# Kernel tuning notes

Hardware: AMD Instinct MI355X
Metric: run time of the kernel (lower is better)

The kernel has to match this reference:

```python
import jax, jax.numpy as jnp
import numpy as np

LATENT_DIM = 16
NUM_REPLICATES = 10
NUM_STEPS = 10
DT = 0.01
# second-order term index pairs (i <= j), matching standard SINDy library ordering
_TRIU_I, _TRIU_J = np.triu_indices(LATENT_DIM)


def sindy_library(z):
    """z: [..., d] -> Theta: [..., 1 + d + d(d+1)/2 + d] (poly_order=2, include_sine=True)."""
    ones = jnp.ones(z.shape[:-1] + (1,), dtype=z.dtype)
    quad = z[..., _TRIU_I] * z[..., _TRIU_J]  # [..., 136]
    return jnp.concatenate([ones, z, quad, jnp.sin(z)], axis=-1)  # [..., 169]


def setup_inputs() -> dict:
    key = jax.random.key(0)
    k1, k2 = jax.random.split(key)
    h_t = jax.random.normal(k1, (50000, LATENT_DIM), dtype=jnp.float32)
    # torch.nn.init.normal_(coefficients, mean=0.0, std=0.001)
    coefficients = jax.random.normal(k2, (NUM_REPLICATES, 169, LATENT_DIM), dtype=jnp.float32) * 0.001
    coefficient_mask = jnp.ones((NUM_REPLICATES, 169, LATENT_DIM), dtype=jnp.float32)
    return {"h_t": h_t, "coefficients": coefficients, "coefficient_mask": coefficient_mask}


def reference(h_t, coefficients, coefficient_mask):
    # ht_replicates = h_t.unsqueeze(1).repeat(1, num_replicates, 1)
    h_rep = jnp.broadcast_to(h_t[:, None, :], (h_t.shape[0], NUM_REPLICATES, LATENT_DIM))
    masked_coeff = coefficients * coefficient_mask  # [r, l, d]
    # 10 sequential Euler integration steps (E_SINDy.forward)
    for _ in range(NUM_STEPS):
        theta = sindy_library(h_rep)  # [n, r, 169]
        h_rep = h_rep + jnp.einsum('nrl,rld->nrd', theta, masked_coeff) * DT
    return h_rep
```

## Files before the change

kernel.cpp:

```cpp
#include <hip/hip_runtime.h>
#include <hip/hip_bf16.h>
#include <math.h>

#define LATENT 16
#define NREP 10
#define NSTEPS 10
#define NTERMS 169
#define NCHUNK 7
#define DT 0.01f
#define ASCALE 1024.0f
#define INV_ASCALE (1.0f/1024.0f)

#define WS_A_BYTES (NREP * NCHUNK * 64 * 16)
#define WS_C0_OFF  WS_A_BYTES
#define WS_TOTAL   (WS_A_BYTES + NREP * LATENT * 4)

typedef _Float16 h2 __attribute__((ext_vector_type(2)));
typedef _Float16 half8 __attribute__((ext_vector_type(8)));
typedef __fp16 fp16x2 __attribute__((ext_vector_type(2)));
typedef __attribute__((ext_vector_type(4))) float f32x4;
typedef int int4v __attribute__((ext_vector_type(4)));

union FragH  { half8 v; h2 p[4]; int4v i4; };
union FragHE { half8 v; _Float16 e[8]; int4v i4; };

#define SW(x) __builtin_shufflevector((x), (x), 1, 0)

__device__ __forceinline__ h2 pkrtz(float a, float b) {
    fp16x2 r = __builtin_amdgcn_cvt_pkrtz(a, b);
    return __builtin_bit_cast(h2, r);
}

__device__ __forceinline__ h2 shfl_xor_h2(h2 v, int mask) {
    int i = __builtin_bit_cast(int, v);
    return __builtin_bit_cast(h2, __shfl_xor(i, mask));
}

__host__ __device__ constexpr int quadrow(int x, int y) {
    if (x > y) { int t = x; x = y; y = t; }
    return 17 + x * 16 - x * (x - 1) / 2 + (y - x);
}

__host__ __device__ constexpr int krow16(int m, int g) {
    const int sh = 4 * g;
    if (m < 4)  return 1 + (m ^ sh);
    if (m < 8)  return 153 + ((m - 4) ^ sh);
    if (m < 12) { const int a = (m - 8) ^ sh; return quadrow(a, a); }
    if (m < 14) { const int u = m - 12; return quadrow((2*u) ^ sh, (2*u+1) ^ sh); }
    if (m < 30) {
        const int idx = m - 14, rep = idx >> 2, w = idx & 3;
        const int v = 2 * rep + 1;
        const int a = ((w == 1 || w == 3) ? 1 : 0);
        const int b = 2 * v + ((w == 1 || w == 2) ? 1 : 0);
        return quadrow(a ^ sh, b ^ sh);
    }
    if (m < 54) {
        const int idx = m - 30, rep = idx >> 2, w = idx & 3;
        const int u = rep & 1;
        const int v = 2 + 2 * (rep >> 1) + (rep & 1);
        const int d = u ^ v;
        const bool live = (d == 2) ? (g == 0 || g == 2) : (g == 0 || g == 1);
        if (!live) return -1;
        const int a = 2 * u + ((w == 1 || w == 3) ? 1 : 0);
        const int b = 2 * v + ((w == 1 || w == 2) ? 1 : 0);
        return quadrow(a ^ sh, b ^ sh);
    }
    return -1;
}

__global__ __launch_bounds__(448) void pack_A16_kernel(
    const float* __restrict__ coeff, const float* __restrict__ mask, char* __restrict__ ws)
{
    const int r = blockIdx.x;
    const int tid = threadIdx.x;
    const int c = tid >> 6, lane = tid & 63;
    const int d = lane & 15, g = lane >> 4;
    const float* cr = coeff + (size_t)r * NTERMS * LATENT;
    const float* mr = mask  + (size_t)r * NTERMS * LATENT;
    FragHE a;
    for (int e = 0; e < 8; ++e) {
        const int row = krow16(c * 8 + e, g);
        float v = 0.0f;
        if (row >= 0) v = cr[row * LATENT + d] * mr[row * LATENT + d] * (DT * ASCALE);
        a.e[e] = (_Float16)v;
    }
    reinterpret_cast<int4v*>(ws)[((size_t)r * NCHUNK + c) * 64 + lane] = a.i4;

    if (tid < LATENT) {
        float* c0p = reinterpret_cast<float*>(ws + WS_C0_OFF);
        c0p[r * LATENT + tid] = cr[tid] * mr[tid] * (DT * ASCALE);
    }
}

template<bool USE_WS>
__global__ __launch_bounds__(256, 4) void sindy_f16_kernel(
    const float* __restrict__ h_t,
    const float* __restrict__ coeff,
    const float* __restrict__ mask,
    const char* __restrict__ ws,
    float* __restrict__ out,
    int N, int ntiles)
{
    const int lane = threadIdx.x & 63;
    const int wid  = blockIdx.x * 4 + (threadIdx.x >> 6);
    if (wid >= NREP * ntiles) return;
    const int r    = wid / ntiles;
    const int tile = wid % ntiles;

    const int col = lane & 15;
    const int g   = lane >> 4;

    int4v afi[NCHUNK];
    if constexpr (USE_WS) {
        const int4v* wa = reinterpret_cast<const int4v*>(ws);
        #pragma unroll
        for (int c = 0; c < NCHUNK; ++c)
            afi[c] = wa[((size_t)r * NCHUNK + c) * 64 + lane];
    } else {
        const float* cr = coeff + (size_t)r * NTERMS * LATENT;
        const float* mr = mask  + (size_t)r * NTERMS * LATENT;
        #pragma unroll
        for (int c = 0; c < NCHUNK; ++c) {
            FragHE a;
            #pragma unroll
            for (int e = 0; e < 8; ++e) {
                const int row = krow16(c * 8 + e, g);
                float v = 0.0f;
                if (row >= 0) v = cr[row * LATENT + col] * mr[row * LATENT + col] * (DT * ASCALE);
                a.e[e] = (_Float16)v;
            }
            afi[c] = a.i4;
        }
    }

    float c0s[4];
    if constexpr (USE_WS) {
        const float4 v = *reinterpret_cast<const float4*>(
            ws + WS_C0_OFF + ((size_t)r * LATENT + 4 * g) * 4);
        c0s[0] = v.x; c0s[1] = v.y; c0s[2] = v.z; c0s[3] = v.w;
    } else {
        const float* cr = coeff + (size_t)r * NTERMS * LATENT;
        const float* mr = mask  + (size_t)r * NTERMS * LATENT;
        #pragma unroll
        for (int j = 0; j < 4; ++j) {
            const int d2 = 4 * g + j;
            c0s[j] = cr[d2] * mr[d2] * (DT * ASCALE);
        }
    }

    #pragma unroll
    for (int c = 0; c < NCHUNK; ++c) asm volatile("" : "+v"(afi[c]));
    asm volatile("" : "+v"(c0s[0]), "+v"(c0s[1]), "+v"(c0s[2]), "+v"(c0s[3]));

    const int n = tile * 16 + col;
    float h0, h1, h2c, h3c;
    {
        float4 q = make_float4(0.f, 0.f, 0.f, 0.f);
        if (n < N)
            q = *reinterpret_cast<const float4*>(h_t + (size_t)n * LATENT + 4 * g);
        h0 = q.x; h1 = q.y; h2c = q.z; h3c = q.w;
    }

    for (int s = 0; s < NSTEPS; ++s) {
        h2 hp[8];
        hp[0] = pkrtz(h0, h1);
        hp[1] = pkrtz(h2c, h3c);
        #pragma unroll
        for (int u = 1; u < 4; ++u) {
            hp[2 * u]     = shfl_xor_h2(hp[0], 16 * u);
            hp[2 * u + 1] = shfl_xor_h2(hp[1], 16 * u);
        }

        f32x4 acc;
        acc[0] = fmaf(h0,  ASCALE, c0s[0]);
        acc[1] = fmaf(h1,  ASCALE, c0s[1]);
        acc[2] = fmaf(h2c, ASCALE, c0s[2]);
        acc[3] = fmaf(h3c, ASCALE, c0s[3]);

        FragH f;
        #define MM(C) acc = __builtin_amdgcn_mfma_f32_16x16x32_f16( \
            __builtin_bit_cast(half8, afi[C]), f.v, acc, 0, 0, 0);
        f.p[0] = hp[0]; f.p[1] = hp[1];
        f.p[2] = pkrtz(__sinf(h0), __sinf(h1));
        f.p[3] = pkrtz(__sinf(h2c), __sinf(h3c));
        MM(0)
        f.p[0] = hp[0] * hp[0]; f.p[1] = hp[1] * hp[1];
        f.p[2] = pkrtz(h0 * h1, h2c * h3c);
        f.p[3] = hp[0] * hp[1];
        MM(1)
        f.p[0] = hp[0] * SW(hp[1]); f.p[1] = hp[0] * hp[3];
        f.p[2] = hp[0] * SW(hp[3]); f.p[3] = hp[0] * hp[5];
        MM(2)
        f.p[0] = hp[0] * SW(hp[5]); f.p[1] = hp[0] * hp[7];
        f.p[2] = hp[0] * SW(hp[7]); f.p[3] = hp[0] * hp[2];
        MM(3)
        f.p[0] = hp[0] * SW(hp[2]); f.p[1] = hp[1] * hp[3];
        f.p[2] = hp[1] * SW(hp[3]); f.p[3] = hp[0] * hp[4];
        MM(4)
        f.p[0] = hp[0] * SW(hp[4]); f.p[1] = hp[1] * hp[5];
        f.p[2] = hp[1] * SW(hp[5]); f.p[3] = hp[0] * hp[6];
        MM(5)
        f.p[0] = hp[0] * SW(hp[6]); f.p[1] = hp[1] * hp[7];
        f.p[2] = hp[1] * SW(hp[7]); f.p[3] = (h2)(_Float16)0;
        MM(6)
        #undef MM

        h0  = acc[0] * INV_ASCALE;
        h1  = acc[1] * INV_ASCALE;
        h2c = acc[2] * INV_ASCALE;
        h3c = acc[3] * INV_ASCALE;
    }

    if (n < N) {
        float* op = out + ((size_t)n * NREP + r) * LATENT + 4 * g;
        *reinterpret_cast<float4*>(op) = make_float4(h0, h1, h2c, h3c);
    }
}

extern "C" void kernel_launch(void* const* d_in, const int* in_sizes, int n_in,
                              void* d_out, int out_size, void* d_ws, size_t ws_size,
                              hipStream_t stream) {
    const float* h_t   = (const float*)d_in[0];
    const float* coeff = (const float*)d_in[1];
    const float* mask  = (const float*)d_in[2];
    float* out = (float*)d_out;

    const int N = in_sizes[0] / LATENT;
    const int ntiles = (N + 15) / 16;
    const int nwaves = NREP * ntiles;
    const int nblocks = (nwaves + 3) / 4;

    if (ws_size >= (size_t)WS_TOTAL) {
        pack_A16_kernel<<<dim3(NREP), dim3(448), 0, stream>>>(coeff, mask, (char*)d_ws);
        sindy_f16_kernel<true><<<dim3(nblocks), dim3(256), 0, stream>>>(
            h_t, coeff, mask, (const char*)d_ws, out, N, ntiles);
    } else {
        sindy_f16_kernel<false><<<dim3(nblocks), dim3(256), 0, stream>>>(
            h_t, coeff, mask, (const char*)d_ws, out, N, ntiles);
    }
}
```

Before: 55.49 us.

## Process two 16-row tiles per wave to interleave independent MFMA chains

Each wave now handles two tiles of 16 samples that share the same coefficient fragments. It alternates MFMAs between two independent accumulators, so one chain's dependency latency can be covered by the other's work. The launch bound drops from 4 to 3 waves per SIMD to make room for the extra registers. The pack kernel is also split into 70 single-wave blocks. The trade-off is fewer resident waves and half as many waves overall, and the asm barriers that pinned fragments in registers are removed.

Result: no change. 55.18 us (-0.6%).

```diff
diff --git a/kernel.cpp b/kernel.cpp
--- a/kernel.cpp
+++ b/kernel.cpp
@@ -68,12 +68,42 @@
     return -1;
 }
 
-__global__ __launch_bounds__(448) void pack_A16_kernel(
+template<int C>
+__device__ __forceinline__ half8 buildf(const float (&hq)[4], const h2 (&hp)[8]) {
+    FragH f;
+    if constexpr (C == 0) {
+        f.p[0] = hp[0]; f.p[1] = hp[1];
+        f.p[2] = pkrtz(__sinf(hq[0]), __sinf(hq[1]));
+        f.p[3] = pkrtz(__sinf(hq[2]), __sinf(hq[3]));
+    } else if constexpr (C == 1) {
+        f.p[0] = hp[0] * hp[0]; f.p[1] = hp[1] * hp[1];
+        f.p[2] = pkrtz(hq[0] * hq[1], hq[2] * hq[3]);
+        f.p[3] = hp[0] * hp[1];
+    } else if constexpr (C == 2) {
+        f.p[0] = hp[0] * SW(hp[1]); f.p[1] = hp[0] * hp[3];
+        f.p[2] = hp[0] * SW(hp[3]); f.p[3] = hp[0] * hp[5];
+    } else if constexpr (C == 3) {
+        f.p[0] = hp[0] * SW(hp[5]); f.p[1] = hp[0] * hp[7];
+        f.p[2] = hp[0] * SW(hp[7]); f.p[3] = hp[0] * hp[2];
+    } else if constexpr (C == 4) {
+        f.p[0] = hp[0] * SW(hp[2]); f.p[1] = hp[1] * hp[3];
+        f.p[2] = hp[1] * SW(hp[3]); f.p[3] = hp[0] * hp[4];
+    } else if constexpr (C == 5) {
+        f.p[0] = hp[0] * SW(hp[4]); f.p[1] = hp[1] * hp[5];
+        f.p[2] = hp[1] * SW(hp[5]); f.p[3] = hp[0] * hp[6];
+    } else {
+        f.p[0] = hp[0] * SW(hp[6]); f.p[1] = hp[1] * hp[7];
+        f.p[2] = hp[1] * SW(hp[7]); f.p[3] = (h2)(_Float16)0;
+    }
+    return f.v;
+}
+
+__global__ __launch_bounds__(64) void pack_A16_kernel(
     const float* __restrict__ coeff, const float* __restrict__ mask, char* __restrict__ ws)
 {
-    const int r = blockIdx.x;
-    const int tid = threadIdx.x;
-    const int c = tid >> 6, lane = tid & 63;
+    const int r = blockIdx.x / NCHUNK;
+    const int c = blockIdx.x % NCHUNK;
+    const int lane = threadIdx.x;
     const int d = lane & 15, g = lane >> 4;
     const float* cr = coeff + (size_t)r * NTERMS * LATENT;
     const float* mr = mask  + (size_t)r * NTERMS * LATENT;
@@ -86,26 +116,26 @@
     }
     reinterpret_cast<int4v*>(ws)[((size_t)r * NCHUNK + c) * 64 + lane] = a.i4;
 
-    if (tid < LATENT) {
+    if (c == 0 && lane < LATENT) {
         float* c0p = reinterpret_cast<float*>(ws + WS_C0_OFF);
-        c0p[r * LATENT + tid] = cr[tid] * mr[tid] * (DT * ASCALE);
+        c0p[r * LATENT + lane] = cr[lane] * mr[lane] * (DT * ASCALE);
     }
 }
 
 template<bool USE_WS>
-__global__ __launch_bounds__(256, 4) void sindy_f16_kernel(
+__global__ __launch_bounds__(256, 3) void sindy_f16_kernel(
     const float* __restrict__ h_t,
     const float* __restrict__ coeff,
     const float* __restrict__ mask,
     const char* __restrict__ ws,
     float* __restrict__ out,
-    int N, int ntiles)
+    int N, int npairs)
 {
     const int lane = threadIdx.x & 63;
     const int wid  = blockIdx.x * 4 + (threadIdx.x >> 6);
-    if (wid >= NREP * ntiles) return;
-    const int r    = wid / ntiles;
-    const int tile = wid % ntiles;
+    if (wid >= NREP * npairs) return;
+    const int r    = wid / npairs;
+    const int pair = wid % npairs;
 
     const int col = lane & 15;
     const int g   = lane >> 4;
@@ -148,72 +178,61 @@
         }
     }
 
-    #pragma unroll
-    for (int c = 0; c < NCHUNK; ++c) asm volatile("" : "+v"(afi[c]));
-    asm volatile("" : "+v"(c0s[0]), "+v"(c0s[1]), "+v"(c0s[2]), "+v"(c0s[3]));
-
-    const int n = tile * 16 + col;
-    float h0, h1, h2c, h3c;
+    const int nA = (2 * pair) * 16 + col;
+    const int nB = nA + 16;
+    float hqA[4], hqB[4];
     {
         float4 q = make_float4(0.f, 0.f, 0.f, 0.f);
-        if (n < N)
-            q = *reinterpret_cast<const float4*>(h_t + (size_t)n * LATENT + 4 * g);
-        h0 = q.x; h1 = q.y; h2c = q.z; h3c = q.w;
+        if (nA < N) q = *reinterpret_cast<const float4*>(h_t + (size_t)nA * LATENT + 4 * g);
+        hqA[0] = q.x; hqA[1] = q.y; hqA[2] = q.z; hqA[3] = q.w;
+        float4 p = make_float4(0.f, 0.f, 0.f, 0.f);
+        if (nB < N) p = *reinterpret_cast<const float4*>(h_t + (size_t)nB * LATENT + 4 * g);
+        hqB[0] = p.x; hqB[1] = p.y; hqB[2] = p.z; hqB[3] = p.w;
     }
 
     for (int s = 0; s < NSTEPS; ++s) {
-        h2 hp[8];
-        hp[0] = pkrtz(h0, h1);
-        hp[1] = pkrtz(h2c, h3c);
+        h2 hpA[8], hpB[8];
+        hpA[0] = pkrtz(hqA[0], hqA[1]); hpA[1] = pkrtz(hqA[2], hqA[3]);
+        hpB[0] = pkrtz(hqB[0], hqB[1]); hpB[1] = pkrtz(hqB[2], hqB[3]);
         #pragma unroll
         for (int u = 1; u < 4; ++u) {
-            hp[2 * u]     = shfl_xor_h2(hp[0], 16 * u);
-            hp[2 * u + 1] = shfl_xor_h2(hp[1], 16 * u);
+            hpA[2 * u]     = shfl_xor_h2(hpA[0], 16 * u);
+            hpA[2 * u + 1] = shfl_xor_h2(hpA[1], 16 * u);
+            hpB[2 * u]     = shfl_xor_h2(hpB[0], 16 * u);
+            hpB[2 * u + 1] = shfl_xor_h2(hpB[1], 16 * u);
         }
 
-        f32x4 acc;
-        acc[0] = fmaf(h0,  ASCALE, c0s[0]);
-        acc[1] = fmaf(h1,  ASCALE, c0s[1]);
-        acc[2] = fmaf(h2c, ASCALE, c0s[2]);
-        acc[3] = fmaf(h3c, ASCALE, c0s[3]);
-
-        FragH f;
-        #define MM(C) acc = __builtin_amdgcn_mfma_f32_16x16x32_f16( \
-            __builtin_bit_cast(half8, afi[C]), f.v, acc, 0, 0, 0);
-        f.p[0] = hp[0]; f.p[1] = hp[1];
-        f.p[2] = pkrtz(__sinf(h0), __sinf(h1));
-        f.p[3] = pkrtz(__sinf(h2c), __sinf(h3c));
-        MM(0)
-        f.p[0] = hp[0] * hp[0]; f.p[1] = hp[1] * hp[1];
-        f.p[2] = pkrtz(h0 * h1, h2c * h3c);
-        f.p[3] = hp[0] * hp[1];
-        MM(1)
-        f.p[0] = hp[0] * SW(hp[1]); f.p[1] = hp[0] * hp[3];
-        f.p[2] = hp[0] * SW(hp[3]); f.p[3] = hp[0] * hp[5];
-        MM(2)
-        f.p[0] = hp[0] * SW(hp[5]); f.p[1] = hp[0] * hp[7];
-        f.p[2] = hp[0] * SW(hp[7]); f.p[3] = hp[0] * hp[2];
-        MM(3)
-        f.p[0] = hp[0] * SW(hp[2]); f.p[1] = hp[1] * hp[3];
-        f.p[2] = hp[1] * SW(hp[3]); f.p[3] = hp[0] * hp[4];
-        MM(4)
-        f.p[0] = hp[0] * SW(hp[4]); f.p[1] = hp[1] * hp[5];
-        f.p[2] = hp[1] * SW(hp[5]); f.p[3] = hp[0] * hp[6];
-        MM(5)
-        f.p[0] = hp[0] * SW(hp[6]); f.p[1] = hp[1] * hp[7];
-        f.p[2] = hp[1] * SW(hp[7]); f.p[3] = (h2)(_Float16)0;
-        MM(6)
-        #undef MM
-
-        h0  = acc[0] * INV_ASCALE;
-        h1  = acc[1] * INV_ASCALE;
-        h2c = acc[2] * INV_ASCALE;
-        h3c = acc[3] * INV_ASCALE;
-    }
-
-    if (n < N) {
-        float* op = out + ((size_t)n * NREP + r) * LATENT + 4 * g;
-        *reinterpret_cast<float4*>(op) = make_float4(h0, h1, h2c, h3c);
+        f32x4 accA, accB;
+        accA[0] = fmaf(hqA[0], ASCALE, c0s[0]);
+        accA[1] = fmaf(hqA[1], ASCALE, c0s[1]);
+        accA[2] = fmaf(hqA[2], ASCALE, c0s[2]);
+        accA[3] = fmaf(hqA[3], ASCALE, c0s[3]);
+        accB[0] = fmaf(hqB[0], ASCALE, c0s[0]);
+        accB[1] = fmaf(hqB[1], ASCALE, c0s[1]);
+        accB[2] = fmaf(hqB[2], ASCALE, c0s[2]);
+        accB[3] = fmaf(hqB[3], ASCALE, c0s[3]);
+
+        #define MMPAIR(C) \
+            accA = __builtin_amdgcn_mfma_f32_16x16x32_f16( \
+                __builtin_bit_cast(half8, afi[C]), buildf<C>(hqA, hpA), accA, 0, 0, 0); \
+            accB = __builtin_amdgcn_mfma_f32_16x16x32_f16( \
+                __builtin_bit_cast(half8, afi[C]), buildf<C>(hqB, hpB), accB, 0, 0, 0);
+        MMPAIR(0) MMPAIR(1) MMPAIR(2) MMPAIR(3) MMPAIR(4) MMPAIR(5) MMPAIR(6)
+        #undef MMPAIR
+
+        hqA[0] = accA[0] * INV_ASCALE; hqA[1] = accA[1] * INV_ASCALE;
+        hqA[2] = accA[2] * INV_ASCALE; hqA[3] = accA[3] * INV_ASCALE;
+        hqB[0] = accB[0] * INV_ASCALE; hqB[1] = accB[1] * INV_ASCALE;
+        hqB[2] = accB[2] * INV_ASCALE; hqB[3] = accB[3] * INV_ASCALE;
+    }
+
+    if (nA < N) {
+        float* op = out + ((size_t)nA * NREP + r) * LATENT + 4 * g;
+        *reinterpret_cast<float4*>(op) = make_float4(hqA[0], hqA[1], hqA[2], hqA[3]);
+    }
+    if (nB < N) {
+        float* op = out + ((size_t)nB * NREP + r) * LATENT + 4 * g;
+        *reinterpret_cast<float4*>(op) = make_float4(hqB[0], hqB[1], hqB[2], hqB[3]);
     }
 }
 
@@ -227,15 +246,16 @@
 
     const int N = in_sizes[0] / LATENT;
     const int ntiles = (N + 15) / 16;
-    const int nwaves = NREP * ntiles;
+    const int npairs = (ntiles + 1) / 2;
+    const int nwaves = NREP * npairs;
     const int nblocks = (nwaves + 3) / 4;
 
     if (ws_size >= (size_t)WS_TOTAL) {
-        pack_A16_kernel<<<dim3(NREP), dim3(448), 0, stream>>>(coeff, mask, (char*)d_ws);
+        pack_A16_kernel<<<dim3(NREP * NCHUNK), dim3(64), 0, stream>>>(coeff, mask, (char*)d_ws);
         sindy_f16_kernel<true><<<dim3(nblocks), dim3(256), 0, stream>>>(
-            h_t, coeff, mask, (const char*)d_ws, out, N, ntiles);
+            h_t, coeff, mask, (const char*)d_ws, out, N, npairs);
     } else {
         sindy_f16_kernel<false><<<dim3(nblocks), dim3(256), 0, stream>>>(
-            h_t, coeff, mask, (const char*)d_ws, out, N, ntiles);
-    }
-}
+            h_t, coeff, mask, (const char*)d_ws, out, N, npairs);
+    }
+}
```
